# Kernel tuning notes

Measured on AMD Instinct MI355X. Metric: run time of the kernel, lower is better.

## Reference

```python
import jax, jax.numpy as jnp
import numpy as np

B, S, D, H = 2, 2048, 1024, 16
DH = D // H
EPS = 1e-5


def _ln(x, g, b):
    m = jnp.mean(x, axis=-1, keepdims=True)
    v = jnp.mean((x - m) ** 2, axis=-1, keepdims=True)
    return (x - m) * jax.lax.rsqrt(v + EPS) * g + b


def setup_inputs() -> dict:
    key = jax.random.key(0)
    ks = jax.random.split(key, 16)
    w = lambda k, shp: jax.random.normal(k, shp, jnp.float32) * 0.02
    return {
        "x": jax.random.normal(ks[0], (B, S, D), jnp.float32),
        # semantic preprocessor: Linear(D,2D) -> ReLU -> Linear(2D,D), residual + LN
        "pW1": w(ks[1], (D, 2 * D)), "pb1": jnp.zeros((2 * D,), jnp.float32),
        "pW2": w(ks[2], (2 * D, D)), "pb2": jnp.zeros((D,), jnp.float32),
        "gp": jnp.ones((D,), jnp.float32), "bp": jnp.zeros((D,), jnp.float32),
        # multi-head attention projections
        "Wq": w(ks[3], (D, D)), "bq": jnp.zeros((D,), jnp.float32),
        "Wk": w(ks[4], (D, D)), "bk": jnp.zeros((D,), jnp.float32),
        "Wv": w(ks[5], (D, D)), "bv": jnp.zeros((D,), jnp.float32),
        "Wo": w(ks[6], (D, D)), "bo": jnp.zeros((D,), jnp.float32),
        "g1": jnp.ones((D,), jnp.float32), "b1": jnp.zeros((D,), jnp.float32),
        # FFN: Linear(D,4D) -> ReLU -> Linear(4D,D)
        "Wf1": w(ks[7], (D, 4 * D)), "bf1": jnp.zeros((4 * D,), jnp.float32),
        "Wf2": w(ks[8], (4 * D, D)), "bf2": jnp.zeros((D,), jnp.float32),
        "g2": jnp.ones((D,), jnp.float32), "b2": jnp.zeros((D,), jnp.float32),
    }


def reference(x, pW1, pb1, pW2, pb2, gp, bp,
              Wq, bq, Wk, bk, Wv, bv, Wo, bo, g1, b1,
              Wf1, bf1, Wf2, bf2, g2, b2):
    # specialized 'semantic' preprocessor (dropout = identity in eval)
    h = jax.nn.relu(x @ pW1 + pb1) @ pW2 + pb2
    s = _ln(x + h, gp, bp)                       # [B,S,D]
    # naive multi-head attention
    q = (s @ Wq + bq).reshape(B, S, H, DH)
    k = (s @ Wk + bk).reshape(B, S, H, DH)
    v = (s @ Wv + bv).reshape(B, S, H, DH)
    scores = jnp.einsum("bqhd,bkhd->bhqk", q, k) / np.sqrt(DH).astype(np.float32)
    attn = jax.nn.softmax(scores, axis=-1)       # [B,H,S,S]
    ctx = jnp.einsum("bhqk,bkhd->bqhd", attn, v).reshape(B, S, D)
    attn_out = ctx @ Wo + bo
    y = _ln(s + attn_out, g1, b1)
    # FFN (dropouts = identity)
    f = jax.nn.relu(y @ Wf1 + bf1) @ Wf2 + bf2
    return _ln(y + f, g2, b2)
```

## Files before the change

### kernel.cpp

```cpp
#include <hip/hip_runtime.h>
#include <cstdint>
#include <cstddef>

typedef _Float16 f16;
typedef _Float16 f16x8 __attribute__((ext_vector_type(8)));
typedef _Float16 f16x4 __attribute__((ext_vector_type(4)));
typedef float    f32x4 __attribute__((ext_vector_type(4)));
typedef float    f32x16 __attribute__((ext_vector_type(16)));
typedef unsigned int uint2v __attribute__((ext_vector_type(2)));

#define MFMA16(a,b,c) __builtin_amdgcn_mfma_f32_16x16x32_f16(a, b, c, 0, 0, 0)
#define MFMA32(a,b,c) __builtin_amdgcn_mfma_f32_32x32x16_f16(a, b, c, 0, 0, 0)

static __device__ __forceinline__ void gload_lds16(const void* g, void* l) {
  __builtin_amdgcn_global_load_lds(
      (const __attribute__((address_space(1))) unsigned int*)g,
      (__attribute__((address_space(3))) unsigned int*)l, 16, 0, 0);
}

static __device__ __forceinline__ int pkh(float a, float b) {
  auto t = __builtin_amdgcn_cvt_pkrtz(a, b);
  return __builtin_bit_cast(int, t);
}

static __device__ __forceinline__ float ex2(float x) {
  return __builtin_amdgcn_exp2f(x);
}

static __device__ __forceinline__ uint2v pswap(int a, int b) {
  return __builtin_amdgcn_permlane32_swap((unsigned)a, (unsigned)b, false, false);
}
static __device__ __forceinline__ float xhalf_max(float x) {
  uint2v r = pswap(__builtin_bit_cast(int, x), __builtin_bit_cast(int, x));
  return fmaxf(__builtin_bit_cast(float, r.x), __builtin_bit_cast(float, r.y));
}
static __device__ __forceinline__ float xhalf_sum(float x) {
  uint2v r = pswap(__builtin_bit_cast(int, x), __builtin_bit_cast(int, x));
  return __builtin_bit_cast(float, r.x) + __builtin_bit_cast(float, r.y);
}

__global__ __launch_bounds__(256) void cast_kernel(const float* __restrict__ x,
                                                   f16* __restrict__ y, int n4) {
  int i = blockIdx.x * 256 + threadIdx.x;
  if (i < n4) {
    float4 v = ((const float4*)x)[i];
    f16x4 h;
    h[0] = (f16)v.x; h[1] = (f16)v.y; h[2] = (f16)v.z; h[3] = (f16)v.w;
    *(f16x4*)(y + (size_t)i * 4) = h;
  }
}

__global__ __launch_bounds__(256) void wtrans(const float* __restrict__ W,
                                              f16* __restrict__ Wt, int K, int N,
                                              float scale) {
  __shared__ float tile[32][33];
  const int n0 = blockIdx.x * 32, k0 = blockIdx.y * 32;
  const int c = threadIdx.x & 31, r = threadIdx.x >> 5;
#pragma unroll
  for (int i = 0; i < 4; i++) {
    int row = r + i * 8;
    tile[row][c] = W[(size_t)(k0 + row) * N + n0 + c];
  }
  __syncthreads();
#pragma unroll
  for (int i = 0; i < 4; i++) {
    int row = r + i * 8;
    Wt[(size_t)(n0 + row) * K + k0 + c] = (f16)(tile[c][row] * scale);
  }
}

__global__ __launch_bounds__(256) void qkvbias_kernel(const float* __restrict__ bq,
                                                      const float* __restrict__ bk,
                                                      const float* __restrict__ bv,
                                                      float* __restrict__ bqkv) {
  int i = blockIdx.x * 256 + threadIdx.x;
  if (i < 1024)       bqkv[i] = bq[i] * 0.18033688f;
  else if (i < 2048)  bqkv[i] = bk[i - 1024];
  else if (i < 3072)  bqkv[i] = bv[i - 2048];
}

template <int MODE, int BN>
__global__ __launch_bounds__(256, 2)
void gemm_kernel(const f16* __restrict__ A, const f16* __restrict__ W,
                 const float* __restrict__ bias, const f16* __restrict__ res,
                 void* __restrict__ out, f16* __restrict__ vt, int N, int K,
                 int gx) {
  __shared__ __align__(16) f16 lsA[128 * 64];
  __shared__ __align__(16) f16 lsB[BN * 64];
  constexpr int MI = (BN == 128) ? 4 : 2;
  constexpr int NB = (BN == 128) ? 4 : 2;
  const int tid  = threadIdx.x;
  const int lane = tid & 63;
  const int wid  = tid >> 6;
  const int frow = lane & 15;
  const int kgrp = lane >> 4;
  const int wmBase = (BN == 128) ? (wid >> 1) * 64 : wid * 32;
  const int wnBase = (BN == 128) ? (wid & 1) * 64 : 0;

  const int bid = blockIdx.x;
  const int xcd = bid & 7, slot = bid >> 3;
  const int bm = (xcd << 2) + slot / gx;
  const int bn = slot % gx;

  const f32x4 zero4 = {0.f, 0.f, 0.f, 0.f};
  f32x4 acc[MI][4];
#pragma unroll
  for (int i = 0; i < MI; i++)
#pragma unroll
    for (int j = 0; j < 4; j++) acc[i][j] = zero4;

  const f16* aSrc[4]; int lOffA[4];
  const f16* bSrc[NB]; int lOffB[NB];
#pragma unroll
  for (int i = 0; i < 4; i++) {
    int c_lin = i * 256 + wid * 64 + lane;
    int row = c_lin >> 3;
    int ch  = (c_lin & 7) ^ (row & 7);
    aSrc[i] = A + (size_t)(bm * 128 + row) * K + ch * 8;
    lOffA[i] = (i * 256 + wid * 64) * 8;
  }
#pragma unroll
  for (int i = 0; i < NB; i++) {
    int c_lin = i * 256 + wid * 64 + lane;
    int row = c_lin >> 3;
    int ch  = (c_lin & 7) ^ (row & 7);
    bSrc[i] = W + (size_t)(bn * BN + row) * K + ch * 8;
    lOffB[i] = (i * 256 + wid * 64) * 8;
  }

  const int nk = K >> 6;
  for (int ks = 0; ks < nk; ++ks) {
#pragma unroll
    for (int i = 0; i < 4; i++) gload_lds16(aSrc[i] + ks * 64, &lsA[lOffA[i]]);
#pragma unroll
    for (int i = 0; i < NB; i++) gload_lds16(bSrc[i] + ks * 64, &lsB[lOffB[i]]);
    __syncthreads();
#pragma unroll
    for (int kk = 0; kk < 2; kk++) {
      f16x8 af[MI], bf[4];
#pragma unroll
      for (int i = 0; i < MI; i++) {
        int row = wmBase + i * 16 + frow;
        af[i] = *(const f16x8*)&lsA[row * 64 + (((kk * 4 + kgrp) ^ (row & 7)) << 3)];
      }
#pragma unroll
      for (int j = 0; j < 4; j++) {
        int row = wnBase + j * 16 + frow;
        bf[j] = *(const f16x8*)&lsB[row * 64 + (((kk * 4 + kgrp) ^ (row & 7)) << 3)];
      }
#pragma unroll
      for (int i = 0; i < MI; i++)
#pragma unroll
        for (int j = 0; j < 4; j++) acc[i][j] = MFMA16(af[i], bf[j], acc[i][j]);
    }
    __syncthreads();
  }

#pragma unroll
  for (int j = 0; j < 4; j++) {
    const int col = bn * BN + wnBase + j * 16 + frow;
    const float bb = bias[col];
#pragma unroll
    for (int i = 0; i < MI; i++) {
      const int row0 = bm * 128 + wmBase + i * 16 + kgrp * 4;
      if (MODE == 3 && col >= 2048) {
        const int vcol = col - 2048;
        const int bh = (row0 >> 11) * 16 + (vcol >> 6);
        const int d  = vcol & 63;
        const int kv = row0 & 2047;
        f16x4 pk;
#pragma unroll
        for (int r = 0; r < 4; r++) pk[r] = (f16)(acc[i][j][r] + bb);
        *(f16x4*)(vt + ((size_t)bh * 64 + d) * 2048 + kv) = pk;
      } else {
#pragma unroll
        for (int r = 0; r < 4; r++) {
          float v = acc[i][j][r] + bb;
          const size_t idx = (size_t)(row0 + r) * N + col;
          if (MODE == 1) v = fmaxf(v, 0.f);
          if (MODE == 2) v += (float)res[idx];
          ((f16*)out)[idx] = (f16)v;
        }
      }
    }
  }
}

__global__ __launch_bounds__(256, 4)
void attn_kernel(const f16* __restrict__ Qp, const f16* __restrict__ Kp,
                 const f16* __restrict__ Vt, f16* __restrict__ opart,
                 float* __restrict__ Lbuf, int ldq) {
  __shared__ __align__(16) f16 lsKb[2 * 64 * 64];
  __shared__ __align__(16) f16 lsVb[2 * 64 * 64];
  const int tid = threadIdx.x, lane = tid & 63, wid = tid >> 6;
  const int qcol = lane & 31;
  const int hi = lane >> 5;
  const int bid = blockIdx.x;
  const int idx = bid >> 3;
  const int bh = ((bid & 7) << 2) | (idx & 3);
  const int rest = idx >> 2;
  const int part = rest & 1;
  const int qt = rest >> 1;
  const int b = bh >> 4, h = bh & 15;
  const size_t rb = (size_t)b * 2048;
  const int hc = h * 64;
  const int kv0 = part * 1024;
  const int qrow = qt * 128 + wid * 32 + qcol;

  f16x8 qf[4];
  {
    const f16* qp = Qp + (rb + qrow) * ldq + hc;
#pragma unroll
    for (int kc = 0; kc < 4; kc++) qf[kc] = *(const f16x8*)(qp + kc * 16 + hi * 8);
  }

  f32x16 ot0, ot1;
#pragma unroll
  for (int i = 0; i < 16; i++) { ot0[i] = 0.f; ot1[i] = 0.f; }
  float mrun = -1e30f, lrun = 0.f;

  const f16 *kS0, *kS1, *vS0, *vS1;
  int off0, off1;
  {
    int c0 = wid * 64 + lane;
    int r0 = c0 >> 3, ch0 = (c0 & 7) ^ (r0 & 7);
    int c1 = 256 + wid * 64 + lane;
    int r1 = c1 >> 3, ch1 = (c1 & 7) ^ (r1 & 7);
    kS0 = Kp + (rb + kv0 + r0) * ldq + hc + ch0 * 8;
    kS1 = Kp + (rb + kv0 + r1) * ldq + hc + ch1 * 8;
    const f16* vbase = Vt + (size_t)bh * 64 * 2048 + kv0;
    vS0 = vbase + (size_t)r0 * 2048 + ch0 * 8;
    vS1 = vbase + (size_t)r1 * 2048 + ch1 * 8;
    off0 = (wid * 64) * 8;
    off1 = (256 + wid * 64) * 8;
  }

#define ASTAGE(T, PB)                                                    \
  {                                                                      \
    f16* kd = lsKb + (PB) * 4096;                                        \
    f16* vd = lsVb + (PB) * 4096;                                        \
    const size_t ko = (size_t)(T) * 64 * ldq;                            \
    const size_t vo = (size_t)(T) * 64;                                  \
    gload_lds16(kS0 + ko, kd + off0);                                    \
    gload_lds16(kS1 + ko, kd + off1);                                    \
    gload_lds16(vS0 + vo, vd + off0);                                    \
    gload_lds16(vS1 + vo, vd + off1);                                    \
  }

  ASTAGE(0, 0);
  asm volatile("s_waitcnt vmcnt(0)" ::: "memory");
  __builtin_amdgcn_s_barrier();

  for (int kt = 0; kt < 16; ++kt) {
    const int cur = kt & 1;
    if (kt < 15) ASTAGE(kt + 1, cur ^ 1);
    const f16* kb = lsKb + cur * 4096;
    const f16* vb = lsVb + cur * 4096;

    f32x16 s0, s1;
#pragma unroll
    for (int i = 0; i < 16; i++) { s0[i] = 0.f; s1[i] = 0.f; }
    const int kr0 = qcol, kr1 = 32 + qcol;
    __builtin_amdgcn_s_setprio(1);
#pragma unroll
    for (int kc = 0; kc < 4; kc++) {
      f16x8 a0 = *(const f16x8*)&kb[kr0 * 64 + (((kc * 2 + hi) ^ (kr0 & 7)) << 3)];
      f16x8 a1 = *(const f16x8*)&kb[kr1 * 64 + (((kc * 2 + hi) ^ (kr1 & 7)) << 3)];
      s0 = MFMA32(a0, qf[kc], s0);
      s1 = MFMA32(a1, qf[kc], s1);
    }
    __builtin_amdgcn_s_setprio(0);

    float mx[16];
#pragma unroll
    for (int r = 0; r < 16; r++) mx[r] = fmaxf(s0[r], s1[r]);
#pragma unroll
    for (int w = 8; w > 0; w >>= 1)
#pragma unroll
      for (int r = 0; r < w; r++) mx[r] = fmaxf(mx[r], mx[r + w]);
    float pmax = xhalf_max(mx[0]);
    if (__any(pmax > mrun + 11.54f)) {
      float mn = fmaxf(mrun, pmax);
      float fac = ex2(mrun - mn);
      mrun = mn;
      lrun *= fac;
#pragma unroll
      for (int i = 0; i < 16; i++) { ot0[i] *= fac; ot1[i] *= fac; }
    }
#pragma unroll
    for (int r = 0; r < 16; r++) {
      s0[r] = ex2(s0[r] - mrun);
      s1[r] = ex2(s1[r] - mrun);
    }
    float sm[16];
#pragma unroll
    for (int r = 0; r < 16; r++) sm[r] = s0[r] + s1[r];
#pragma unroll
    for (int w = 8; w > 0; w >>= 1)
#pragma unroll
      for (int r = 0; r < w; r++) sm[r] += sm[r + w];
    lrun += xhalf_sum(sm[0]);

#pragma unroll
    for (int st = 0; st < 2; ++st) {
#pragma unroll
      for (int c0 = 0; c0 < 2; c0++) {
        const int c8 = c0 * 8;
        int a0, a1, b0, b1;
        if (st == 0) {
          a0 = pkh(s0[c8 + 0], s0[c8 + 1]); a1 = pkh(s0[c8 + 2], s0[c8 + 3]);
          b0 = pkh(s0[c8 + 4], s0[c8 + 5]); b1 = pkh(s0[c8 + 6], s0[c8 + 7]);
        } else {
          a0 = pkh(s1[c8 + 0], s1[c8 + 1]); a1 = pkh(s1[c8 + 2], s1[c8 + 3]);
          b0 = pkh(s1[c8 + 4], s1[c8 + 5]); b1 = pkh(s1[c8 + 6], s1[c8 + 7]);
        }
        uint2v r0 = pswap(a0, b0);
        uint2v r1 = pswap(a1, b1);
        int4 wv;
        wv.x = (int)r0.x; wv.y = (int)r1.x; wv.z = (int)r0.y; wv.w = (int)r1.y;
        f16x8 pfrag = __builtin_bit_cast(f16x8, wv);
        const int ch = st * 4 + c0 * 2 + hi;
        const int vr0 = qcol, vr1 = 32 + qcol;
        f16x8 av0 = *(const f16x8*)&vb[vr0 * 64 + ((ch ^ (vr0 & 7)) << 3)];
        f16x8 av1 = *(const f16x8*)&vb[vr1 * 64 + ((ch ^ (vr1 & 7)) << 3)];
        __builtin_amdgcn_s_setprio(1);
        ot0 = MFMA32(av0, pfrag, ot0);
        ot1 = MFMA32(av1, pfrag, ot1);
        __builtin_amdgcn_s_setprio(0);
      }
    }
    asm volatile("s_waitcnt vmcnt(0)" ::: "memory");
    __builtin_amdgcn_s_barrier();
  }
#undef ASTAGE

  const float rinv = 1.f / lrun;
  const size_t pbase = ((size_t)part * 32 + bh) * 2048 + qrow;
  f16* pp = opart + pbase * 64;
#pragma unroll
  for (int rr = 0; rr < 16; rr += 2) {
    const int d = (rr & 3) + 8 * (rr >> 2) + 4 * hi;
    *(int*)(pp + d)      = pkh(ot0[rr] * rinv, ot0[rr + 1] * rinv);
    *(int*)(pp + 32 + d) = pkh(ot1[rr] * rinv, ot1[rr + 1] * rinv);
  }
  if (hi == 0) Lbuf[pbase] = mrun + __builtin_amdgcn_logf(lrun);
}

__global__ __launch_bounds__(256)
void combine_kernel(const f16* __restrict__ opart, const float* __restrict__ Lbuf,
                    f16* __restrict__ ctx) {
  const int bid = blockIdx.x;
  const int bh = bid >> 5, qblk = bid & 31;
  const int t = threadIdx.x;
  const int q = qblk * 64 + (t >> 2);
  const int dp = (t & 3) * 16;
  const size_t base = (size_t)bh * 2048 + q;
  const size_t p1o = (size_t)32 * 2048;
  const float L0 = Lbuf[base];
  const float L1 = Lbuf[p1o + base];
  const float L = fmaxf(L0, L1);
  float w0 = ex2(L0 - L), w1 = ex2(L1 - L);
  const float rs = 1.f / (w0 + w1);
  w0 *= rs; w1 *= rs;
  const f16* p0 = opart + base * 64 + dp;
  const f16* p1 = opart + (p1o + base) * 64 + dp;
  f16x8 a0 = *(const f16x8*)p0, a1 = *(const f16x8*)(p0 + 8);
  f16x8 c0 = *(const f16x8*)p1, c1 = *(const f16x8*)(p1 + 8);
  f16x8 o0, o1;
#pragma unroll
  for (int j = 0; j < 8; j++) {
    o0[j] = (f16)(w0 * (float)a0[j] + w1 * (float)c0[j]);
    o1[j] = (f16)(w0 * (float)a1[j] + w1 * (float)c1[j]);
  }
  const int b = bh >> 4, h = bh & 15;
  f16* op = ctx + ((size_t)b * 2048 + q) * 1024 + h * 64 + dp;
  *(f16x8*)op = o0;
  *(f16x8*)(op + 8) = o1;
}

__global__ __launch_bounds__(256)
void ln_kernel(const f16* __restrict__ x, const float* __restrict__ g,
               const float* __restrict__ be, float* __restrict__ of,
               f16* __restrict__ ob) {
  const int row = blockIdx.x, t = threadIdx.x;
  const f16x4 h4 = *(const f16x4*)(x + (size_t)row * 1024 + t * 4);
  float v0 = (float)h4[0], v1 = (float)h4[1], v2 = (float)h4[2], v3 = (float)h4[3];
  float s = v0 + v1 + v2 + v3;
  float q = v0 * v0 + v1 * v1 + v2 * v2 + v3 * v3;
#pragma unroll
  for (int off = 1; off < 64; off <<= 1) {
    s += __shfl_xor(s, off);
    q += __shfl_xor(q, off);
  }
  __shared__ float ss[4], sq[4];
  if ((t & 63) == 0) { ss[t >> 6] = s; sq[t >> 6] = q; }
  __syncthreads();
  s = ss[0] + ss[1] + ss[2] + ss[3];
  q = sq[0] + sq[1] + sq[2] + sq[3];
  const float mean = s * (1.f / 1024.f);
  const float var  = q * (1.f / 1024.f) - mean * mean;
  const float rstd = rsqrtf(var + 1e-5f);
  const float4 gv = ((const float4*)g)[t];
  const float4 bv = ((const float4*)be)[t];
  float4 ov;
  ov.x = (v0 - mean) * rstd * gv.x + bv.x;
  ov.y = (v1 - mean) * rstd * gv.y + bv.y;
  ov.z = (v2 - mean) * rstd * gv.z + bv.z;
  ov.w = (v3 - mean) * rstd * gv.w + bv.w;
  if (of) ((float4*)(of + (size_t)row * 1024))[t] = ov;
  if (ob) {
    f16x4 hv;
    hv[0] = (f16)ov.x; hv[1] = (f16)ov.y; hv[2] = (f16)ov.z; hv[3] = (f16)ov.w;
    *(f16x4*)(ob + (size_t)row * 1024 + t * 4) = hv;
  }
}

extern "C" void kernel_launch(void* const* d_in, const int* in_sizes, int n_in,
                              void* d_out, int out_size, void* d_ws, size_t ws_size,
                              hipStream_t stream) {
  const float* x   = (const float*)d_in[0];
  const float* pW1 = (const float*)d_in[1];
  const float* pb1 = (const float*)d_in[2];
  const float* pW2 = (const float*)d_in[3];
  const float* pb2 = (const float*)d_in[4];
  const float* gp  = (const float*)d_in[5];
  const float* bp  = (const float*)d_in[6];
  const float* Wq  = (const float*)d_in[7];
  const float* bq  = (const float*)d_in[8];
  const float* Wk  = (const float*)d_in[9];
  const float* bk  = (const float*)d_in[10];
  const float* Wv  = (const float*)d_in[11];
  const float* bv  = (const float*)d_in[12];
  const float* Wo  = (const float*)d_in[13];
  const float* bo  = (const float*)d_in[14];
  const float* g1  = (const float*)d_in[15];
  const float* b1  = (const float*)d_in[16];
  const float* Wf1 = (const float*)d_in[17];
  const float* bf1 = (const float*)d_in[18];
  const float* Wf2 = (const float*)d_in[19];
  const float* bf2 = (const float*)d_in[20];
  const float* g2  = (const float*)d_in[21];
  const float* b2  = (const float*)d_in[22];

  char* ws = (char*)d_ws;
  const size_t MB = 1024 * 1024;
  if (ws_size < 121 * MB) return;

  f16*   wtP1 = (f16*)(ws);
  f16*   wtP2 = (f16*)(ws + 4 * MB);
  f16*   wtQ  = (f16*)(ws + 8 * MB);
  f16*   wtO  = (f16*)(ws + 14 * MB);
  f16*   wtF1 = (f16*)(ws + 16 * MB);
  f16*   wtF2 = (f16*)(ws + 24 * MB);
  f16*   big  = (f16*)(ws + 32 * MB);
  f16*   xb   = (f16*)(ws + 64 * MB);
  f16*   tb   = (f16*)(ws + 72 * MB);
  f16*   sb   = (f16*)(ws + 80 * MB);
  f16*   ybuf = (f16*)(ws + 88 * MB);
  f16*   ctx  = (f16*)(ws + 96 * MB);
  f16*   opart= (f16*)(ws + 104 * MB);
  float* Lbuf = (float*)(ws + 120 * MB);
  float* bqkv = (float*)(ws + 120 * MB + 512 * 1024);
  f16*   wtK  = wtQ + (size_t)1024 * 1024;
  f16*   wtV  = wtQ + (size_t)2048 * 1024;
  f16*   Vt   = big + (size_t)4096 * 3072;

  dim3 blk(256);
  qkvbias_kernel<<<12, blk, 0, stream>>>(bq, bk, bv, bqkv);
  cast_kernel<<<4096, blk, 0, stream>>>(x, xb, 1048576);
  wtrans<<<dim3(64, 32),  blk, 0, stream>>>(pW1, wtP1, 1024, 2048, 1.f);
  wtrans<<<dim3(32, 64),  blk, 0, stream>>>(pW2, wtP2, 2048, 1024, 1.f);
  wtrans<<<dim3(32, 32),  blk, 0, stream>>>(Wq,  wtQ,  1024, 1024, 0.18033688f);
  wtrans<<<dim3(32, 32),  blk, 0, stream>>>(Wk,  wtK,  1024, 1024, 1.f);
  wtrans<<<dim3(32, 32),  blk, 0, stream>>>(Wv,  wtV,  1024, 1024, 1.f);
  wtrans<<<dim3(32, 32),  blk, 0, stream>>>(Wo,  wtO,  1024, 1024, 1.f);
  wtrans<<<dim3(128, 32), blk, 0, stream>>>(Wf1, wtF1, 1024, 4096, 1.f);
  wtrans<<<dim3(32, 128), blk, 0, stream>>>(Wf2, wtF2, 4096, 1024, 1.f);

  gemm_kernel<1,128><<<512, blk, 0, stream>>>(xb, wtP1, pb1, nullptr, big, nullptr, 2048, 1024, 16);
  gemm_kernel<2,64><<<512, blk, 0, stream>>>(big, wtP2, pb2, xb, tb, nullptr, 1024, 2048, 16);
  ln_kernel<<<4096, blk, 0, stream>>>(tb, gp, bp, nullptr, sb);
  gemm_kernel<3,128><<<768, blk, 0, stream>>>(sb, wtQ, bqkv, nullptr, big, Vt, 3072, 1024, 24);
  attn_kernel<<<1024, blk, 0, stream>>>(big, big + 1024, Vt, opart, Lbuf, 3072);
  combine_kernel<<<1024, blk, 0, stream>>>(opart, Lbuf, ctx);
  gemm_kernel<2,64><<<512, blk, 0, stream>>>(ctx, wtO, bo, sb, tb, nullptr, 1024, 1024, 16);
  ln_kernel<<<4096, blk, 0, stream>>>(tb, g1, b1, nullptr, ybuf);
  gemm_kernel<1,128><<<1024, blk, 0, stream>>>(ybuf, wtF1, bf1, nullptr, big, nullptr, 4096, 1024, 32);
  gemm_kernel<2,64><<<512, blk, 0, stream>>>(big, wtF2, bf2, ybuf, tb, nullptr, 1024, 4096, 16);
  ln_kernel<<<4096, blk, 0, stream>>>(tb, g2, b2, (float*)d_out, nullptr);
}
```

Baseline: 309.7 us.

## Replace narrow-tile N=1024 GEMMs with split-K 128x128 tiles, fuse reduction into LayerNorm

The three GEMMs with N=1024 (preproc second linear, output projection, FFN second linear) previously used 128x64 tiles with the bias and residual applied in the epilogue. They now use a split-K kernel with 128x128 tiles and two K halves, each writing its fp16 partial to a workspace buffer. A new LayerNorm kernel sums the two partials, adds bias and residual, then normalizes. This raises per-block MFMA reuse while keeping the block count at 512, at the cost of writing and reading an extra partial buffer and storing each partial in fp16.

```diff
diff --git a/kernel.cpp b/kernel.cpp
--- a/kernel.cpp
+++ b/kernel.cpp
@@ -79,23 +79,20 @@
   else if (i < 3072)  bqkv[i] = bv[i - 2048];
 }
 
-template <int MODE, int BN>
+template <int MODE>
 __global__ __launch_bounds__(256, 2)
 void gemm_kernel(const f16* __restrict__ A, const f16* __restrict__ W,
-                 const float* __restrict__ bias, const f16* __restrict__ res,
-                 void* __restrict__ out, f16* __restrict__ vt, int N, int K,
-                 int gx) {
+                 const float* __restrict__ bias, void* __restrict__ out,
+                 f16* __restrict__ vt, int N, int K, int gx) {
   __shared__ __align__(16) f16 lsA[128 * 64];
-  __shared__ __align__(16) f16 lsB[BN * 64];
-  constexpr int MI = (BN == 128) ? 4 : 2;
-  constexpr int NB = (BN == 128) ? 4 : 2;
+  __shared__ __align__(16) f16 lsB[128 * 64];
   const int tid  = threadIdx.x;
   const int lane = tid & 63;
   const int wid  = tid >> 6;
   const int frow = lane & 15;
   const int kgrp = lane >> 4;
-  const int wmBase = (BN == 128) ? (wid >> 1) * 64 : wid * 32;
-  const int wnBase = (BN == 128) ? (wid & 1) * 64 : 0;
+  const int wmBase = (wid >> 1) * 64;
+  const int wnBase = (wid & 1) * 64;
 
   const int bid = blockIdx.x;
   const int xcd = bid & 7, slot = bid >> 3;
@@ -103,29 +100,23 @@
   const int bn = slot % gx;
 
   const f32x4 zero4 = {0.f, 0.f, 0.f, 0.f};
-  f32x4 acc[MI][4];
-#pragma unroll
-  for (int i = 0; i < MI; i++)
+  f32x4 acc[4][4];
+#pragma unroll
+  for (int i = 0; i < 4; i++)
 #pragma unroll
     for (int j = 0; j < 4; j++) acc[i][j] = zero4;
 
   const f16* aSrc[4]; int lOffA[4];
-  const f16* bSrc[NB]; int lOffB[NB];
+  const f16* bSrc[4]; int lOffB[4];
 #pragma unroll
   for (int i = 0; i < 4; i++) {
     int c_lin = i * 256 + wid * 64 + lane;
     int row = c_lin >> 3;
     int ch  = (c_lin & 7) ^ (row & 7);
     aSrc[i] = A + (size_t)(bm * 128 + row) * K + ch * 8;
+    bSrc[i] = W + (size_t)(bn * 128 + row) * K + ch * 8;
     lOffA[i] = (i * 256 + wid * 64) * 8;
-  }
-#pragma unroll
-  for (int i = 0; i < NB; i++) {
-    int c_lin = i * 256 + wid * 64 + lane;
-    int row = c_lin >> 3;
-    int ch  = (c_lin & 7) ^ (row & 7);
-    bSrc[i] = W + (size_t)(bn * BN + row) * K + ch * 8;
-    lOffB[i] = (i * 256 + wid * 64) * 8;
+    lOffB[i] = lOffA[i];
   }
 
   const int nk = K >> 6;
@@ -133,13 +124,13 @@
 #pragma unroll
     for (int i = 0; i < 4; i++) gload_lds16(aSrc[i] + ks * 64, &lsA[lOffA[i]]);
 #pragma unroll
-    for (int i = 0; i < NB; i++) gload_lds16(bSrc[i] + ks * 64, &lsB[lOffB[i]]);
+    for (int i = 0; i < 4; i++) gload_lds16(bSrc[i] + ks * 64, &lsB[lOffB[i]]);
     __syncthreads();
 #pragma unroll
     for (int kk = 0; kk < 2; kk++) {
-      f16x8 af[MI], bf[4];
-#pragma unroll
-      for (int i = 0; i < MI; i++) {
+      f16x8 af[4], bf[4];
+#pragma unroll
+      for (int i = 0; i < 4; i++) {
         int row = wmBase + i * 16 + frow;
         af[i] = *(const f16x8*)&lsA[row * 64 + (((kk * 4 + kgrp) ^ (row & 7)) << 3)];
       }
@@ -149,7 +140,7 @@
         bf[j] = *(const f16x8*)&lsB[row * 64 + (((kk * 4 + kgrp) ^ (row & 7)) << 3)];
       }
 #pragma unroll
-      for (int i = 0; i < MI; i++)
+      for (int i = 0; i < 4; i++)
 #pragma unroll
         for (int j = 0; j < 4; j++) acc[i][j] = MFMA16(af[i], bf[j], acc[i][j]);
     }
@@ -158,10 +149,10 @@
 
 #pragma unroll
   for (int j = 0; j < 4; j++) {
-    const int col = bn * BN + wnBase + j * 16 + frow;
+    const int col = bn * 128 + wnBase + j * 16 + frow;
     const float bb = bias[col];
 #pragma unroll
-    for (int i = 0; i < MI; i++) {
+    for (int i = 0; i < 4; i++) {
       const int row0 = bm * 128 + wmBase + i * 16 + kgrp * 4;
       if (MODE == 3 && col >= 2048) {
         const int vcol = col - 2048;
@@ -176,13 +167,138 @@
 #pragma unroll
         for (int r = 0; r < 4; r++) {
           float v = acc[i][j][r] + bb;
-          const size_t idx = (size_t)(row0 + r) * N + col;
           if (MODE == 1) v = fmaxf(v, 0.f);
-          if (MODE == 2) v += (float)res[idx];
-          ((f16*)out)[idx] = (f16)v;
+          ((f16*)out)[(size_t)(row0 + r) * N + col] = (f16)v;
         }
       }
     }
+  }
+}
+
+__global__ __launch_bounds__(256, 2)
+void gemm_splitk(const f16* __restrict__ A, const f16* __restrict__ W,
+                 f16* __restrict__ outp, int K) {
+  __shared__ __align__(16) f16 lsA[128 * 64];
+  __shared__ __align__(16) f16 lsB[128 * 64];
+  const int tid  = threadIdx.x;
+  const int lane = tid & 63;
+  const int wid  = tid >> 6;
+  const int frow = lane & 15;
+  const int kgrp = lane >> 4;
+  const int wmBase = (wid >> 1) * 64;
+  const int wnBase = (wid & 1) * 64;
+
+  const int bid = blockIdx.x;
+  const int xcd = bid & 7, slot = bid >> 3;
+  const int q = slot >> 3, bn = slot & 7;
+  const int bmkp = xcd * 8 + q;
+  const int bm = bmkp >> 1, kp = bmkp & 1;
+  const int Kh = K >> 1;
+  const f16* Ab = A + kp * Kh;
+  const f16* Wb = W + kp * Kh;
+
+  const f32x4 zero4 = {0.f, 0.f, 0.f, 0.f};
+  f32x4 acc[4][4];
+#pragma unroll
+  for (int i = 0; i < 4; i++)
+#pragma unroll
+    for (int j = 0; j < 4; j++) acc[i][j] = zero4;
+
+  const f16* aSrc[4]; const f16* bSrc[4]; int lOff[4];
+#pragma unroll
+  for (int i = 0; i < 4; i++) {
+    int c_lin = i * 256 + wid * 64 + lane;
+    int row = c_lin >> 3;
+    int ch  = (c_lin & 7) ^ (row & 7);
+    aSrc[i] = Ab + (size_t)(bm * 128 + row) * K + ch * 8;
+    bSrc[i] = Wb + (size_t)(bn * 128 + row) * K + ch * 8;
+    lOff[i] = (i * 256 + wid * 64) * 8;
+  }
+
+  const int nk = Kh >> 6;
+  for (int ks = 0; ks < nk; ++ks) {
+#pragma unroll
+    for (int i = 0; i < 4; i++) gload_lds16(aSrc[i] + ks * 64, &lsA[lOff[i]]);
+#pragma unroll
+    for (int i = 0; i < 4; i++) gload_lds16(bSrc[i] + ks * 64, &lsB[lOff[i]]);
+    __syncthreads();
+#pragma unroll
+    for (int kk = 0; kk < 2; kk++) {
+      f16x8 af[4], bf[4];
+#pragma unroll
+      for (int i = 0; i < 4; i++) {
+        int row = wmBase + i * 16 + frow;
+        af[i] = *(const f16x8*)&lsA[row * 64 + (((kk * 4 + kgrp) ^ (row & 7)) << 3)];
+      }
+#pragma unroll
+      for (int j = 0; j < 4; j++) {
+        int row = wnBase + j * 16 + frow;
+        bf[j] = *(const f16x8*)&lsB[row * 64 + (((kk * 4 + kgrp) ^ (row & 7)) << 3)];
+      }
+#pragma unroll
+      for (int i = 0; i < 4; i++)
+#pragma unroll
+        for (int j = 0; j < 4; j++) acc[i][j] = MFMA16(af[i], bf[j], acc[i][j]);
+    }
+    __syncthreads();
+  }
+
+  f16* op = outp + (size_t)kp * 4096 * 1024;
+#pragma unroll
+  for (int j = 0; j < 4; j++) {
+    const int col = bn * 128 + wnBase + j * 16 + frow;
+#pragma unroll
+    for (int i = 0; i < 4; i++) {
+      const int row0 = bm * 128 + wmBase + i * 16 + kgrp * 4;
+#pragma unroll
+      for (int r = 0; r < 4; r++)
+        op[(size_t)(row0 + r) * 1024 + col] = (f16)acc[i][j][r];
+    }
+  }
+}
+
+__global__ __launch_bounds__(256)
+void ln_res2(const f16* __restrict__ p, const f16* __restrict__ res,
+             const float* __restrict__ bias, const float* __restrict__ g,
+             const float* __restrict__ be, float* __restrict__ of,
+             f16* __restrict__ ob) {
+  const int row = blockIdx.x, t = threadIdx.x;
+  const size_t off = (size_t)row * 1024 + t * 4;
+  const f16x4 a = *(const f16x4*)(p + off);
+  const f16x4 b = *(const f16x4*)(p + (size_t)4096 * 1024 + off);
+  const f16x4 rr = *(const f16x4*)(res + off);
+  const float4 bb = ((const float4*)bias)[t];
+  float v0 = (float)a[0] + (float)b[0] + bb.x + (float)rr[0];
+  float v1 = (float)a[1] + (float)b[1] + bb.y + (float)rr[1];
+  float v2 = (float)a[2] + (float)b[2] + bb.z + (float)rr[2];
+  float v3 = (float)a[3] + (float)b[3] + bb.w + (float)rr[3];
+  float s = v0 + v1 + v2 + v3;
+  float q = v0 * v0 + v1 * v1 + v2 * v2 + v3 * v3;
+#pragma unroll
+  for (int o = 1; o < 64; o <<= 1) {
+    s += __shfl_xor(s, o);
+    q += __shfl_xor(q, o);
+  }
+  __shared__ float ss[4], sq[4];
+  if ((t & 63) == 0) { ss[t >> 6] = s; sq[t >> 6] = q; }
+  __syncthreads();
+  s = ss[0] + ss[1] + ss[2] + ss[3];
+  q = sq[0] + sq[1] + sq[2] + sq[3];
+  const float mean = s * (1.f / 1024.f);
+  const float var  = q * (1.f / 1024.f) - mean * mean;
+  const float rstd = rsqrtf(var + 1e-5f);
+  const float4 gv = ((const float4*)g)[t];
+  const float4 bv = ((const float4*)be)[t];
+  float4 ov;
+  ov.x = (v0 - mean) * rstd * gv.x + bv.x;
+  ov.y = (v1 - mean) * rstd * gv.y + bv.y;
+  ov.z = (v2 - mean) * rstd * gv.z + bv.z;
+  ov.w = (v3 - mean) * rstd * gv.w + bv.w;
+  if (of) ((float4*)(of + (size_t)row * 1024))[t] = ov;
+  if (ob) {
+    f16x4 hv;
+    hv[0] = (f16)ov.x; hv[1] = (f16)ov.y; hv[2] = (f16)ov.z; hv[3] = (f16)ov.w;
+    *(f16x4*)(ob + off) = hv;
   }
 }
 
@@ -376,43 +492,6 @@
   f16* op = ctx + ((size_t)b * 2048 + q) * 1024 + h * 64 + dp;
   *(f16x8*)op = o0;
   *(f16x8*)(op + 8) = o1;
-}
-
-__global__ __launch_bounds__(256)
-void ln_kernel(const f16* __restrict__ x, const float* __restrict__ g,
-               const float* __restrict__ be, float* __restrict__ of,
-               f16* __restrict__ ob) {
-  const int row = blockIdx.x, t = threadIdx.x;
-  const f16x4 h4 = *(const f16x4*)(x + (size_t)row * 1024 + t * 4);
-  float v0 = (float)h4[0], v1 = (float)h4[1], v2 = (float)h4[2], v3 = (float)h4[3];
-  float s = v0 + v1 + v2 + v3;
-  float q = v0 * v0 + v1 * v1 + v2 * v2 + v3 * v3;
-#pragma unroll
-  for (int off = 1; off < 64; off <<= 1) {
-    s += __shfl_xor(s, off);
-    q += __shfl_xor(q, off);
-  }
-  __shared__ float ss[4], sq[4];
-  if ((t & 63) == 0) { ss[t >> 6] = s; sq[t >> 6] = q; }
-  __syncthreads();
-  s = ss[0] + ss[1] + ss[2] + ss[3];
-  q = sq[0] + sq[1] + sq[2] + sq[3];
-  const float mean = s * (1.f / 1024.f);
-  const float var  = q * (1.f / 1024.f) - mean * mean;
-  const float rstd = rsqrtf(var + 1e-5f);
-  const float4 gv = ((const float4*)g)[t];
-  const float4 bv = ((const float4*)be)[t];
-  float4 ov;
-  ov.x = (v0 - mean) * rstd * gv.x + bv.x;
-  ov.y = (v1 - mean) * rstd * gv.y + bv.y;
-  ov.z = (v2 - mean) * rstd * gv.z + bv.z;
-  ov.w = (v3 - mean) * rstd * gv.w + bv.w;
-  if (of) ((float4*)(of + (size_t)row * 1024))[t] = ov;
-  if (ob) {
-    f16x4 hv;
-    hv[0] = (f16)ov.x; hv[1] = (f16)ov.y; hv[2] = (f16)ov.z; hv[3] = (f16)ov.w;
-    *(f16x4*)(ob + (size_t)row * 1024 + t * 4) = hv;
-  }
 }
 
 extern "C" void kernel_launch(void* const* d_in, const int* in_sizes, int n_in,
@@ -454,13 +533,13 @@
   f16*   wtF2 = (f16*)(ws + 24 * MB);
   f16*   big  = (f16*)(ws + 32 * MB);
   f16*   xb   = (f16*)(ws + 64 * MB);
-  f16*   tb   = (f16*)(ws + 72 * MB);
-  f16*   sb   = (f16*)(ws + 80 * MB);
-  f16*   ybuf = (f16*)(ws + 88 * MB);
-  f16*   ctx  = (f16*)(ws + 96 * MB);
-  f16*   opart= (f16*)(ws + 104 * MB);
-  float* Lbuf = (float*)(ws + 120 * MB);
-  float* bqkv = (float*)(ws + 120 * MB + 512 * 1024);
+  f16*   sb   = (f16*)(ws + 72 * MB);
+  f16*   ybuf = (f16*)(ws + 80 * MB);
+  f16*   ctx  = (f16*)(ws + 88 * MB);
+  f16*   part = (f16*)(ws + 96 * MB);
+  f16*   opart= (f16*)(ws + 96 * MB);
+  float* Lbuf = (float*)(ws + 112 * MB);
+  float* bqkv = (float*)(ws + 112 * MB + 512 * 1024);
   f16*   wtK  = wtQ + (size_t)1024 * 1024;
   f16*   wtV  = wtQ + (size_t)2048 * 1024;
   f16*   Vt   = big + (size_t)4096 * 3072;
@@ -477,15 +556,15 @@
   wtrans<<<dim3(128, 32), blk, 0, stream>>>(Wf1, wtF1, 1024, 4096, 1.f);
   wtrans<<<dim3(32, 128), blk, 0, stream>>>(Wf2, wtF2, 4096, 1024, 1.f);
 
-  gemm_kernel<1,128><<<512, blk, 0, stream>>>(xb, wtP1, pb1, nullptr, big, nullptr, 2048, 1024, 16);
-  gemm_kernel<2,64><<<512, blk, 0, stream>>>(big, wtP2, pb2, xb, tb, nullptr, 1024, 2048, 16);
-  ln_kernel<<<4096, blk, 0, stream>>>(tb, gp, bp, nullptr, sb);
-  gemm_kernel<3,128><<<768, blk, 0, stream>>>(sb, wtQ, bqkv, nullptr, big, Vt, 3072, 1024, 24);
+  gemm_kernel<1><<<512, blk, 0, stream>>>(xb, wtP1, pb1, big, nullptr, 2048, 1024, 16);
+  gemm_splitk<<<512, blk, 0, stream>>>(big, wtP2, part, 2048);
+  ln_res2<<<4096, blk, 0, stream>>>(part, xb, pb2, gp, bp, nullptr, sb);
+  gemm_kernel<3><<<768, blk, 0, stream>>>(sb, wtQ, bqkv, big, Vt, 3072, 1024, 24);
   attn_kernel<<<1024, blk, 0, stream>>>(big, big + 1024, Vt, opart, Lbuf, 3072);
   combine_kernel<<<1024, blk, 0, stream>>>(opart, Lbuf, ctx);
-  gemm_kernel<2,64><<<512, blk, 0, stream>>>(ctx, wtO, bo, sb, tb, nullptr, 1024, 1024, 16);
-  ln_kernel<<<4096, blk, 0, stream>>>(tb, g1, b1, nullptr, ybuf);
-  gemm_kernel<1,128><<<1024, blk, 0, stream>>>(ybuf, wtF1, bf1, nullptr, big, nullptr, 4096, 1024, 32);
-  gemm_kernel<2,64><<<512, blk, 0, stream>>>(big, wtF2, bf2, ybuf, tb, nullptr, 1024, 4096, 16);
-  ln_kernel<<<4096, blk, 0, stream>>>(tb, g2, b2, (float*)d_out, nullptr);
-}
+  gemm_splitk<<<512, blk, 0, stream>>>(ctx, wtO, part, 1024);
+  ln_res2<<<4096, blk, 0, stream>>>(part, sb, bo, g1, b1, nullptr, ybuf);
+  gemm_kernel<1><<<1024, blk, 0, stream>>>(ybuf, wtF1, bf1, big, nullptr, 4096, 1024, 32);
+  gemm_splitk<<<512, blk, 0, stream>>>(big, wtF2, part, 4096);
+  ln_res2<<<4096, blk, 0, stream>>>(part, ybuf, bf2, g2, b2, (float*)d_out, nullptr);
+}
```

Measured after the change: 288.9 us. 1.07x faster.
